# Performance work log

Measured on AMD Instinct MI355X. Metric: run time of the kernel, lower is better.

The kernel has to match this reference:

```python
import jax, jax.numpy as jnp
import numpy as np

NUM_LESION_CLS = 8
MAX_INST = 64          # instance ids in mask_gt are < MAX_INST
SIZE_TH = 100.0
# merge_classes=[[1],...,[8]] -> zero-based groups [0..7] => identity merge


def setup_inputs() -> dict:
    key = jax.random.key(0)
    k1, k2, k3 = jax.random.split(key, 3)
    B, H, W, K = 32, 1024, 1024, 64
    pred_class = jax.random.normal(k1, (B, NUM_LESION_CLS), dtype=jnp.float32)
    mask_gt = jax.random.randint(k2, (B, H, W), 0, MAX_INST, dtype=jnp.int32)
    label_gt = jax.random.randint(k3, (B, K, 2), 0, 32, dtype=jnp.int64)
    return {"pred_class": pred_class, "mask_gt": mask_gt, "label_gt": label_gt}


def reference(pred_class, mask_gt, label_gt):
    # Per-sample histogram of instance-id pixel counts: [B, MAX_INST]
    inst_sizes = jax.vmap(lambda m: jnp.bincount(m.reshape(-1), length=MAX_INST))(mask_gt)
    inst_ids = label_gt[..., 0]            # [B, K]
    labels = label_gt[..., 1]              # [B, K]
    sizes = jnp.take_along_axis(inst_sizes, inst_ids, axis=1).astype(jnp.float32)  # [B, K]
    valid = (labels > 0) & (labels <= NUM_LESION_CLS)                              # [B, K]
    # scatter sizes into per-class counts: cnts[b, label-1] += size (if valid)
    onehot = jax.nn.one_hot(jnp.where(valid, labels - 1, 0), NUM_LESION_CLS,
                            dtype=jnp.float32) * valid[..., None].astype(jnp.float32)
    cnts = jnp.einsum('bk,bkc->bc', sizes, onehot)                                 # [B, C]
    # merge_classes is identity here, so class_label == cnts groups
    class_label = jnp.minimum(cnts / SIZE_TH, 1.0)
    # BCEWithLogitsLoss (mean reduction), numerically stable form
    x = pred_class
    loss = jnp.mean(jnp.maximum(x, 0.0) - x * class_label + jnp.log1p(jnp.exp(-jnp.abs(x))))
    return loss
```

## Files before the change

### kernel.cpp

```cpp
#include <hip/hip_runtime.h>
#include <math.h>

#define NB 32
#define HW (1024 * 1024)
#define BINS 64
#define KLBL 64
#define NCLS 8
#define BPI 64
#define TPB 256
#define CHUNK4 4096

__global__ __launch_bounds__(TPB) void hist_kernel(const int* __restrict__ mask,
                                                   int* __restrict__ hist) {
    __shared__ int sh[4][BINS];
    const int tid = threadIdx.x;
    const int b = blockIdx.x / BPI;
    const int part = blockIdx.x % BPI;
    const int wave = tid >> 6;

    sh[tid >> 6][tid & 63] = 0;
    __syncthreads();

    const int4* __restrict__ p4 =
        (const int4*)(mask + (size_t)b * HW) + (size_t)part * CHUNK4;

    #pragma unroll
    for (int h = 0; h < 2; ++h) {
        int4 v[8];
        #pragma unroll
        for (int k = 0; k < 8; ++k)
            v[k] = p4[(h * 8 + k) * TPB + tid];
        #pragma unroll
        for (int k = 0; k < 8; ++k) {
            atomicAdd(&sh[wave][v[k].x & 63], 1);
            atomicAdd(&sh[wave][v[k].y & 63], 1);
            atomicAdd(&sh[wave][v[k].z & 63], 1);
            atomicAdd(&sh[wave][v[k].w & 63], 1);
        }
    }
    __syncthreads();

    if (tid < BINS) {
        int s = sh[0][tid] + sh[1][tid] + sh[2][tid] + sh[3][tid];
        atomicAdd(&hist[b * BINS + tid], s);
    }
}

__global__ __launch_bounds__(TPB) void finalize_kernel(const float* __restrict__ pred,
                                                       const int* __restrict__ lg,
                                                       const int* __restrict__ hist,
                                                       float* __restrict__ out) {
    __shared__ float cnts[NB * NCLS];
    __shared__ float wsum[4];
    const int tid = threadIdx.x;

    cnts[tid] = 0.0f;
    __syncthreads();

    for (int e = tid; e < NB * KLBL; e += TPB) {
        int inst  = lg[e * 2 + 0];
        int label = lg[e * 2 + 1];
        if (label > 0 && label <= NCLS) {
            float sz = (float)hist[(e >> 6) * BINS + (inst & 63)];
            atomicAdd(&cnts[(e >> 6) * NCLS + (label - 1)], sz);
        }
    }
    __syncthreads();

    float x = pred[tid];
    float t = fminf(cnts[tid] * (1.0f / 100.0f), 1.0f);
    float l = fmaxf(x, 0.0f) - x * t + log1pf(expf(-fabsf(x)));

    for (int off = 32; off > 0; off >>= 1)
        l += __shfl_down(l, off, 64);
    if ((tid & 63) == 0) wsum[tid >> 6] = l;
    __syncthreads();
    if (tid == 0)
        out[0] = (wsum[0] + wsum[1] + wsum[2] + wsum[3]) * (1.0f / (NB * NCLS));
}

extern "C" void kernel_launch(void* const* d_in, const int* in_sizes, int n_in,
                              void* d_out, int out_size, void* d_ws, size_t ws_size,
                              hipStream_t stream) {
    const float* pred = (const float*)d_in[0];
    const int*   mask = (const int*)d_in[1];
    const int*   lg   = (const int*)d_in[2];
    float* out = (float*)d_out;
    int* hist = (int*)d_ws;

    hipMemsetAsync(hist, 0, NB * BINS * sizeof(int), stream);
    hist_kernel<<<NB * BPI, TPB, 0, stream>>>(mask, hist);
    finalize_kernel<<<1, TPB, 0, stream>>>(pred, lg, hist, out);
}
```

Baseline: 203.7 us.

## Stream mask via async global-to-LDS loads and count pixel pairs in 2D table

Rewrites the histogram kernel to prefetch mask data straight into LDS with global_load_lds in a 4-deep software pipeline. Each thread now does one atomic per pair of pixels, into a 64x64 pair-count table, which halves the LDS atomic count. The table is then reduced by row and column sums into per-bin totals. Block count is halved so each block covers more data. The risks are the larger LDS footprint (16KB table plus staging), which lowers occupancy, and hand-written vmcnt waits that depend on the exact number of loads in flight.

```diff
diff --git a/kernel.cpp b/kernel.cpp
--- a/kernel.cpp
+++ b/kernel.cpp
@@ -6,44 +6,76 @@
 #define BINS 64
 #define KLBL 64
 #define NCLS 8
-#define BPI 64
 #define TPB 256
-#define CHUNK4 4096
+#define BPI 32
+#define NBLK (NB * BPI)
+#define STG 64
+#define NST 32
+#define DEPTH 4
 
 __global__ __launch_bounds__(TPB) void hist_kernel(const int* __restrict__ mask,
                                                    int* __restrict__ hist) {
-    __shared__ int sh[4][BINS];
+    __shared__ int4 stage[DEPTH][4][STG];
+    __shared__ unsigned int table[BINS * BINS];
+    __shared__ unsigned int h64[BINS];
+
     const int tid = threadIdx.x;
-    const int b = blockIdx.x / BPI;
-    const int part = blockIdx.x % BPI;
-    const int wave = tid >> 6;
+    const int wave = tid >> 6, lane = tid & 63;
 
-    sh[tid >> 6][tid & 63] = 0;
-    __syncthreads();
-
-    const int4* __restrict__ p4 =
-        (const int4*)(mask + (size_t)b * HW) + (size_t)part * CHUNK4;
-
-    #pragma unroll
-    for (int h = 0; h < 2; ++h) {
-        int4 v[8];
+    {
+        uint4* z = (uint4*)table;
         #pragma unroll
-        for (int k = 0; k < 8; ++k)
-            v[k] = p4[(h * 8 + k) * TPB + tid];
-        #pragma unroll
-        for (int k = 0; k < 8; ++k) {
-            atomicAdd(&sh[wave][v[k].x & 63], 1);
-            atomicAdd(&sh[wave][v[k].y & 63], 1);
-            atomicAdd(&sh[wave][v[k].z & 63], 1);
-            atomicAdd(&sh[wave][v[k].w & 63], 1);
-        }
+        for (int i = 0; i < (BINS * BINS / 4) / TPB; ++i)
+            z[i * TPB + tid] = make_uint4(0u, 0u, 0u, 0u);
+        if (tid < BINS) h64[tid] = 0u;
     }
     __syncthreads();
 
-    if (tid < BINS) {
-        int s = sh[0][tid] + sh[1][tid] + sh[2][tid] + sh[3][tid];
-        atomicAdd(&hist[b * BINS + tid], s);
+    const int b = blockIdx.x >> 5, r = blockIdx.x & 31;
+    const int4* gw = (const int4*)(mask + (size_t)b * HW)
+                   + (size_t)r * (4 * NST * STG) + wave * (NST * STG) + lane;
+
+    auto issue = [&](int s) {
+        __builtin_amdgcn_global_load_lds(
+            (const __attribute__((address_space(1))) void*)(gw + s * STG),
+            (__attribute__((address_space(3))) void*)&stage[s & (DEPTH - 1)][wave][0],
+            16, 0, 0);
+    };
+    auto consume = [&](int s) {
+        int4 v = stage[s & (DEPTH - 1)][wave][lane];
+        atomicAdd(&table[((v.x & 63) << 6) | (v.y & 63)], 1u);
+        atomicAdd(&table[((v.z & 63) << 6) | (v.w & 63)], 1u);
+    };
+
+    #pragma unroll
+    for (int k = 0; k < DEPTH; ++k) issue(k);
+
+    #pragma unroll 4
+    for (int s = 0; s < NST - DEPTH; ++s) {
+        asm volatile("s_waitcnt vmcnt(3)" ::: "memory");
+        __builtin_amdgcn_sched_barrier(0);
+        consume(s);
+        issue(s + DEPTH);
     }
+    asm volatile("s_waitcnt vmcnt(0)" ::: "memory");
+    __builtin_amdgcn_sched_barrier(0);
+    #pragma unroll
+    for (int s = NST - DEPTH; s < NST; ++s) consume(s);
+
+    __syncthreads();
+
+    unsigned int acc = 0;
+    {
+        const uint4* tr = (const uint4*)&table[(tid >> 2) * BINS + (tid & 3) * 16];
+        #pragma unroll
+        for (int j = 0; j < 4; ++j) { uint4 u = tr[j]; acc += u.x + u.y + u.z + u.w; }
+        #pragma unroll
+        for (int j = 0; j < 16; ++j)
+            acc += table[((tid & 3) * 16 + j) * BINS + (tid >> 2)];
+    }
+    atomicAdd(&h64[tid >> 2], acc);
+    __syncthreads();
+    if (tid < BINS) atomicAdd(&hist[b * BINS + tid], (int)h64[tid]);
 }
 
 __global__ __launch_bounds__(TPB) void finalize_kernel(const float* __restrict__ pred,
@@ -89,6 +121,6 @@
     int* hist = (int*)d_ws;
 
     hipMemsetAsync(hist, 0, NB * BINS * sizeof(int), stream);
-    hist_kernel<<<NB * BPI, TPB, 0, stream>>>(mask, hist);
+    hist_kernel<<<NBLK, TPB, 0, stream>>>(mask, hist);
     finalize_kernel<<<1, TPB, 0, stream>>>(pred, lg, hist, out);
 }
```

Result: no change. 202.0 us (-0.8%).
